# Performance work log

Measured on AMD Instinct MI355X. Metric: run time of the kernel, lower is better.

The kernel has to match this reference:

```python
import jax, jax.numpy as jnp
import numpy as np

EPS = 1e-08


def setup_inputs() -> dict:
    key = jax.random.key(0)
    k1, k2, k3 = jax.random.split(key, 3)
    B_img, B_txt, D = 8192, 8192, 512
    img_feature = jax.random.normal(k1, (B_img, D), dtype=jnp.float32)
    text_feature = jax.random.normal(k2, (B_txt, D), dtype=jnp.float32)
    text_lens = jax.random.randint(k3, (B_txt,), 1, 40, dtype=jnp.int32)
    return {"img_feature": img_feature, "text_feature": text_feature, "text_lens": text_lens}


def reference(img_feature, text_feature, text_lens):
    # Pairwise cosine similarity: equivalent to the original expand+mul+sum,
    # expressed as a GEMM of the raw features followed by norm division.
    # w12[i,j] = <img_i, txt_j>; sim = w12 / max(|img_i|*|txt_j|, eps)
    w12 = jnp.einsum('id,jd->ij', img_feature, text_feature)  # [B_img, B_txt]
    w1 = jnp.linalg.norm(img_feature, axis=-1)                # [B_img]
    w2 = jnp.linalg.norm(text_feature, axis=-1)               # [B_txt]
    denom = jnp.maximum(w1[:, None] * w2[None, :], EPS)
    return w12 / denom
```

## Files before the change

### kernel.cpp

```cpp
#include <hip/hip_runtime.h>
#include <hip/hip_bf16.h>

#define M 8192
#define N 8192
#define K 512
#define BM 256
#define BN 128
#define BK 32
#define NT (K / BK)
#define EPSV 1e-8f

typedef __attribute__((ext_vector_type(8))) short bf16x8;
typedef __attribute__((ext_vector_type(4))) float f32x4;
typedef __attribute__((ext_vector_type(8))) unsigned short us8;

__device__ inline void gload_lds16(const void* g, void* l) {
  __builtin_amdgcn_global_load_lds(
      (const __attribute__((address_space(1))) unsigned int*)g,
      (__attribute__((address_space(3))) unsigned int*)l, 16, 0, 0);
}

#define BARRIER()                          \
  do {                                     \
    asm volatile("" ::: "memory");         \
    __builtin_amdgcn_s_barrier();          \
    asm volatile("" ::: "memory");         \
  } while (0)

__global__ __launch_bounds__(256) void prep_kernel(const float* __restrict__ img,
                                                   const float* __restrict__ txt,
                                                   unsigned short* __restrict__ Abf,
                                                   unsigned short* __restrict__ Bbf,
                                                   float* __restrict__ w1,
                                                   float* __restrict__ w2) {
  const int half = blockIdx.x >> 11;
  const int lb = blockIdx.x & 2047;
  const float* in = half ? txt : img;
  unsigned short* outb = half ? Bbf : Abf;
  float* norms = half ? w2 : w1;

  const int gw = (lb * 256 + threadIdx.x) >> 6;
  const int lane = threadIdx.x & 63;
  const float4* rp4 = (const float4*)(in + (size_t)gw * K);
  float4 v0 = rp4[lane * 2];
  float4 v1 = rp4[lane * 2 + 1];
  float ss = v0.x * v0.x + v0.y * v0.y + v0.z * v0.z + v0.w * v0.w +
             v1.x * v1.x + v1.y * v1.y + v1.z * v1.z + v1.w * v1.w;
  float f[8] = {v0.x, v0.y, v0.z, v0.w, v1.x, v1.y, v1.z, v1.w};
  us8 o;
#pragma unroll
  for (int i = 0; i < 8; ++i) {
    __hip_bfloat16 b = __float2bfloat16(f[i]);
    o[i] = *(unsigned short*)&b;
  }
  *(us8*)(outb + (size_t)gw * K + lane * 8) = o;
#pragma unroll
  for (int off = 32; off > 0; off >>= 1) ss += __shfl_down(ss, off, 64);
  if (lane == 0) norms[gw] = 1.0f / fmaxf(sqrtf(ss), 1e-4f);
}

__global__ __launch_bounds__(512, 4) void gemm_kernel(const unsigned short* __restrict__ A,
                                                      const unsigned short* __restrict__ B,
                                                      const float* __restrict__ iw1,
                                                      const float* __restrict__ iw2,
                                                      float* __restrict__ C) {
  __shared__ __align__(128) unsigned short As[2][BM * BK];
  __shared__ __align__(128) unsigned short Bs[3][BN * BK];

  const int tid = threadIdx.x;
  const int wave = tid >> 6;
  const int lane = tid & 63;
  const int wr = wave >> 1;
  const int wc = wave & 1;
  const int fr = lane & 15;
  const int fq = lane >> 4;

  const int xcd = blockIdx.x & 7;
  const int idx = blockIdx.x >> 3;
  const int bRow = (idx >> 3) * BM;
  const int bCol = (xcd * 8 + (idx & 7)) * BN;

  const int srow = lane >> 2;
  const int scol = (lane & 3) * 8;

  auto stageA = [&](int buf, int kt) {
#pragma unroll
    for (int c = 0; c < 2; ++c)
      gload_lds16(A + (size_t)(bRow + c * 128 + wave * 16 + srow) * K + kt * BK + scol,
                  (char*)&As[buf][0] + (c * 128 + wave * 16) * 64);
  };
  auto stageB = [&](int buf, int kt) {
    gload_lds16(B + (size_t)(bCol + wave * 16 + srow) * K + kt * BK + scol,
                (char*)&Bs[buf][0] + wave * 16 * 64);
  };
  auto ldA = [&](int buf, int r) -> bf16x8 {
    return *(const bf16x8*)((const char*)&As[buf][0] + r * 64 + fq * 16);
  };
  auto ldB = [&](int buf, int r) -> bf16x8 {
    return *(const bf16x8*)((const char*)&Bs[buf][0] + r * 64 + fq * 16);
  };

  f32x4 acc[4][4] = {};

  stageA(0, 0);
  stageB(0, 0);
  stageB(1, 1);
  asm volatile("s_waitcnt vmcnt(1)" ::: "memory");
  BARRIER();

#pragma unroll
  for (int t = 0; t < NT; ++t) {
    const int cur = t & 1, nxt = cur ^ 1;
    const int bc = t % 3, b2 = (t + 2) % 3;

    if (t + 1 < NT) stageA(nxt, t + 1);
    if (t + 2 < NT) stageB(b2, t + 2);

    bf16x8 a[4], b[4];
#pragma unroll
    for (int m = 0; m < 4; ++m) a[m] = ldA(cur, wr * 64 + m * 16 + fr);
#pragma unroll
    for (int n = 0; n < 4; ++n) b[n] = ldB(bc, wc * 64 + n * 16 + fr);

    __builtin_amdgcn_s_setprio(1);
#pragma unroll
    for (int m = 0; m < 4; ++m)
#pragma unroll
      for (int n = 0; n < 4; ++n)
        acc[m][n] = __builtin_amdgcn_mfma_f32_16x16x32_bf16(a[m], b[n], acc[m][n], 0, 0, 0);
    __builtin_amdgcn_s_setprio(0);

    if (t < NT - 2) {
      asm volatile("s_waitcnt vmcnt(1)" ::: "memory");
    } else if (t == NT - 2) {
      asm volatile("s_waitcnt vmcnt(0)" ::: "memory");
    }
    BARRIER();
  }

  float i1v[4][4], i2v[4];
#pragma unroll
  for (int m = 0; m < 4; ++m)
#pragma unroll
    for (int r = 0; r < 4; ++r) i1v[m][r] = iw1[bRow + wr * 64 + m * 16 + fq * 4 + r];
#pragma unroll
  for (int n = 0; n < 4; ++n) i2v[n] = iw2[bCol + wc * 64 + n * 16 + fr];

#pragma unroll
  for (int m = 0; m < 4; ++m) {
    const int row0 = bRow + wr * 64 + m * 16 + fq * 4;
#pragma unroll
    for (int n = 0; n < 4; ++n) {
      const int col = bCol + wc * 64 + n * 16 + fr;
      f32x4 v = acc[m][n];
#pragma unroll
      for (int r = 0; r < 4; ++r)
        C[(size_t)(row0 + r) * N + col] = v[r] * i1v[m][r] * i2v[n];
    }
  }
}

extern "C" void kernel_launch(void* const* d_in, const int* in_sizes, int n_in,
                              void* d_out, int out_size, void* d_ws, size_t ws_size,
                              hipStream_t stream) {
  (void)in_sizes; (void)n_in; (void)out_size; (void)ws_size;
  const float* img = (const float*)d_in[0];
  const float* txt = (const float*)d_in[1];
  float* out = (float*)d_out;

  unsigned short* Abf = (unsigned short*)d_ws;
  unsigned short* Bbf = Abf + (size_t)M * K;
  float* w1 = (float*)(Bbf + (size_t)N * K);
  float* w2 = w1 + M;

  prep_kernel<<<4096, 256, 0, stream>>>(img, txt, Abf, Bbf, w1, w2);
  gemm_kernel<<<(M / BM) * (N / BN), 512, 0, stream>>>(Abf, Bbf, w1, w2, out);
}
```

Before: 109.2 us.

## Make GEMM persistent over 8 column tiles and overlap epilogue stores with next tile

```diff
diff --git a/kernel.cpp b/kernel.cpp
--- a/kernel.cpp
+++ b/kernel.cpp
@@ -7,8 +7,8 @@
 #define BM 256
 #define BN 128
 #define BK 32
-#define NT (K / BK)
-#define EPSV 1e-8f
+#define NS 16
+#define NTILE 8
 
 typedef __attribute__((ext_vector_type(8))) short bf16x8;
 typedef __attribute__((ext_vector_type(4))) float f32x4;
@@ -19,6 +19,8 @@
       (const __attribute__((address_space(1))) unsigned int*)g,
       (__attribute__((address_space(3))) unsigned int*)l, 16, 0, 0);
 }
+
+#define MEMFENCE() asm volatile("" ::: "memory")
 
 #define BARRIER()                          \
   do {                                     \
@@ -59,7 +61,7 @@
   if (lane == 0) norms[gw] = 1.0f / fmaxf(sqrtf(ss), 1e-4f);
 }
 
-__global__ __launch_bounds__(512, 4) void gemm_kernel(const unsigned short* __restrict__ A,
+__global__ __launch_bounds__(512, 2) void gemm_kernel(const unsigned short* __restrict__ A,
                                                       const unsigned short* __restrict__ B,
                                                       const float* __restrict__ iw1,
                                                       const float* __restrict__ iw2,
@@ -76,21 +78,22 @@
   const int fq = lane >> 4;
 
   const int xcd = blockIdx.x & 7;
-  const int idx = blockIdx.x >> 3;
-  const int bRow = (idx >> 3) * BM;
-  const int bCol = (xcd * 8 + (idx & 7)) * BN;
+  const int kk = blockIdx.x >> 3;
+  const int bRow = (xcd * 4 + (kk >> 3)) * BM;
+  const int c0 = kk & 7;
+  auto colOf = [&](int t) { return (c0 + 8 * t) * BN; };
 
   const int srow = lane >> 2;
   const int scol = (lane & 3) * 8;
 
-  auto stageA = [&](int buf, int kt) {
+  auto stageA = [&](int buf, int sl) {
 #pragma unroll
     for (int c = 0; c < 2; ++c)
-      gload_lds16(A + (size_t)(bRow + c * 128 + wave * 16 + srow) * K + kt * BK + scol,
+      gload_lds16(A + (size_t)(bRow + c * 128 + wave * 16 + srow) * K + sl * BK + scol,
                   (char*)&As[buf][0] + (c * 128 + wave * 16) * 64);
   };
-  auto stageB = [&](int buf, int kt) {
-    gload_lds16(B + (size_t)(bCol + wave * 16 + srow) * K + kt * BK + scol,
+  auto stageB = [&](int buf, int bCol, int sl) {
+    gload_lds16(B + (size_t)(bCol + wave * 16 + srow) * K + sl * BK + scol,
                 (char*)&Bs[buf][0] + wave * 16 * 64);
   };
   auto ldA = [&](int buf, int r) -> bf16x8 {
@@ -100,62 +103,91 @@
     return *(const bf16x8*)((const char*)&Bs[buf][0] + r * 64 + fq * 16);
   };
 
-  f32x4 acc[4][4] = {};
+  float i1v[4][4];
+#pragma unroll
+  for (int m = 0; m < 4; ++m)
+#pragma unroll
+    for (int r = 0; r < 4; ++r) i1v[m][r] = iw1[bRow + wr * 64 + m * 16 + fq * 4 + r];
+
+  f32x4 accA[4][4] = {}, accB[4][4] = {};
+  float i2A[4] = {}, i2B[4] = {};
 
   stageA(0, 0);
-  stageB(0, 0);
-  stageB(1, 1);
+  stageB(0, colOf(0), 0);
+  stageB(1, colOf(0), 1);
   asm volatile("s_waitcnt vmcnt(1)" ::: "memory");
   BARRIER();
 
-#pragma unroll
-  for (int t = 0; t < NT; ++t) {
-    const int cur = t & 1, nxt = cur ^ 1;
-    const int bc = t % 3, b2 = (t + 2) % 3;
-
-    if (t + 1 < NT) stageA(nxt, t + 1);
-    if (t + 2 < NT) stageB(b2, t + 2);
-
-    bf16x8 a[4], b[4];
-#pragma unroll
-    for (int m = 0; m < 4; ++m) a[m] = ldA(cur, wr * 64 + m * 16 + fr);
-#pragma unroll
-    for (int n = 0; n < 4; ++n) b[n] = ldB(bc, wc * 64 + n * 16 + fr);
-
-    __builtin_amdgcn_s_setprio(1);
+  auto tile_body = [&](f32x4 (&acc)[4][4], float (&i2)[4],
+                       f32x4 (&prev)[4][4], float (&i2p)[4],
+                       int t, int colCur, int colPrev, bool last) {
+#pragma unroll
+    for (int n = 0; n < 4; ++n) i2[n] = iw2[colCur + wc * 64 + n * 16 + fr];
 #pragma unroll
     for (int m = 0; m < 4; ++m)
 #pragma unroll
-      for (int n = 0; n < 4; ++n)
-        acc[m][n] = __builtin_amdgcn_mfma_f32_16x16x32_bf16(a[m], b[n], acc[m][n], 0, 0, 0);
-    __builtin_amdgcn_s_setprio(0);
-
-    if (t < NT - 2) {
-      asm volatile("s_waitcnt vmcnt(1)" ::: "memory");
-    } else if (t == NT - 2) {
-      asm volatile("s_waitcnt vmcnt(0)" ::: "memory");
+      for (int n = 0; n < 4; ++n) acc[m][n] = (f32x4){0.f, 0.f, 0.f, 0.f};
+
+#pragma unroll
+    for (int s = 0; s < NS; ++s) {
+      const int cur = s & 1, nxt = cur ^ 1;
+      const int g = t * NS + s;
+
+      stageA(nxt, (s + 1) & 15);
+      if (!last || s < 14) {
+        const int g2 = g + 2;
+        stageB(g2 % 3, (c0 + 8 * (g2 >> 4)) * BN, g2 & 15);
+      }
+      MEMFENCE();
+      {
+        const int dm = s >> 2, dn = s & 3;
+        const int col = colPrev + wc * 64 + dn * 16 + fr;
+        const int row0 = bRow + wr * 64 + dm * 16 + fq * 4;
+#pragma unroll
+        for (int r = 0; r < 4; ++r)
+          C[(size_t)(row0 + r) * N + col] = prev[dm][dn][r] * i1v[dm][r] * i2p[dn];
+      }
+
+      bf16x8 a[4], b[4];
+#pragma unroll
+      for (int m = 0; m < 4; ++m) a[m] = ldA(cur, wr * 64 + m * 16 + fr);
+      const int bc = g % 3;
+#pragma unroll
+      for (int n = 0; n < 4; ++n) b[n] = ldB(bc, wc * 64 + n * 16 + fr);
+
+      __builtin_amdgcn_s_setprio(1);
+#pragma unroll
+      for (int m = 0; m < 4; ++m)
+#pragma unroll
+        for (int n = 0; n < 4; ++n)
+          acc[m][n] = __builtin_amdgcn_mfma_f32_16x16x32_bf16(a[m], b[n], acc[m][n], 0, 0, 0);
+      __builtin_amdgcn_s_setprio(0);
+
+      if (!last || s < 14) {
+        asm volatile("s_waitcnt vmcnt(5)" ::: "memory");
+      } else if (s == 14) {
+        asm volatile("s_waitcnt vmcnt(4)" ::: "memory");
+      }
+      BARRIER();
     }
-    BARRIER();
+  };
+
+#pragma clang loop unroll(disable)
+  for (int p = 0; p < 4; ++p) {
+    const int tE = 2 * p, tO = 2 * p + 1;
+    tile_body(accA, i2A, accB, i2B, tE, colOf(tE), p ? colOf(tE - 1) : colOf(7), false);
+    tile_body(accB, i2B, accA, i2A, tO, colOf(tO), colOf(tE), tO == 7);
   }
 
-  float i1v[4][4], i2v[4];
-#pragma unroll
-  for (int m = 0; m < 4; ++m)
-#pragma unroll
-    for (int r = 0; r < 4; ++r) i1v[m][r] = iw1[bRow + wr * 64 + m * 16 + fq * 4 + r];
-#pragma unroll
-  for (int n = 0; n < 4; ++n) i2v[n] = iw2[bCol + wc * 64 + n * 16 + fr];
-
-#pragma unroll
-  for (int m = 0; m < 4; ++m) {
-    const int row0 = bRow + wr * 64 + m * 16 + fq * 4;
-#pragma unroll
-    for (int n = 0; n < 4; ++n) {
-      const int col = bCol + wc * 64 + n * 16 + fr;
-      f32x4 v = acc[m][n];
+#pragma unroll
+  for (int dm = 0; dm < 4; ++dm) {
+    const int row0 = bRow + wr * 64 + dm * 16 + fq * 4;
+#pragma unroll
+    for (int dn = 0; dn < 4; ++dn) {
+      const int col = colOf(7) + wc * 64 + dn * 16 + fr;
 #pragma unroll
       for (int r = 0; r < 4; ++r)
-        C[(size_t)(row0 + r) * N + col] = v[r] * i1v[m][r] * i2v[n];
+        C[(size_t)(row0 + r) * N + col] = accB[dm][dn][r] * i1v[dm][r] * i2B[dn];
     }
   }
 }
@@ -174,5 +206,5 @@
   float* w2 = w1 + M;
 
   prep_kernel<<<4096, 256, 0, stream>>>(img, txt, Abf, Bbf, w1, w2);
-  gemm_kernel<<<(M / BM) * (N / BN), 512, 0, stream>>>(Abf, Bbf, w1, w2, out);
-}
+  gemm_kernel<<<256, 512, 0, stream>>>(Abf, Bbf, w1, w2, out);
+}
```

Result: slower. 217.1 us (+98.9%).
